# Kernel optimization log

Hardware: AMD Instinct MI355X
Metric: run time of the kernel (lower is better)

Reference implementation:

```python
import jax, jax.numpy as jnp
import numpy as np

B, N, F, P = 8, 16384, 128, 28


def setup_inputs() -> dict:
    key = jax.random.key(0)
    k1, k2 = jax.random.split(key)
    x = jax.random.uniform(k1, (B, N, 2), dtype=jnp.float32)  # 2D coords in [0,1]
    sigma = jnp.full((1,), np.log(0.05), dtype=jnp.float32)   # learned log-lengthscale
    image_features = jax.random.normal(k2, (F, P, P), dtype=jnp.float32) / np.sqrt(F)
    return {"x": x, "sigma": sigma, "image_features": image_features}


def reference(x, sigma, image_features):
    # x: [B, N, 2], sigma: [1] (log lengthscale), image_features: [F, P, P]
    P_ = image_features.shape[-1]
    grid = jnp.linspace(0.001, 1.0 - 0.001, P_, dtype=x.dtype)  # [P]
    ls = jnp.exp(sigma[0])                                      # lengthscale
    inv = 0.5 / (ls * ls)
    # pairwise squared dists grid vs each coordinate axis -> [B, P, N]
    d0 = (grid[None, :, None] - x[:, None, :, 0]) ** 2
    d1 = (grid[None, :, None] - x[:, None, :, 1]) ** 2
    k0 = jnp.exp(-inv * d0)  # [B, P, N]
    k1 = jnp.exp(-inv * d1)  # [B, P, N]
    # features[b,n,f] = sum_{p,q} k0[b,p,n] * IF[f,p,q] * k1[b,q,n]
    feats = jnp.einsum('bpn,fpq,bqn->bnf', k0, image_features, k1)
    return feats
```

## Files before the change

### kernel.cpp

```cpp
#include <hip/hip_runtime.h>

#define BDIM  8
#define NDIM  16384
#define FDIM  128
#define PDIM  28
#define KPAD  896
#define MPTS  (BDIM * NDIM)

typedef _Float16 half8  __attribute__((ext_vector_type(8)));
typedef float    floatx4 __attribute__((ext_vector_type(4)));

__global__ __launch_bounds__(256) void prep_ift(const float* __restrict__ IF,
                                                _Float16* __restrict__ IFt) {
    int idx = blockIdx.x * 256 + threadIdx.x;
    int f = idx / KPAD;
    int k = idx - f * KPAD;
    int p = k >> 5;
    int q = k & 31;
    float v = (q < PDIM) ? IF[f * (PDIM * PDIM) + p * PDIM + q] : 0.0f;
    IFt[idx] = (_Float16)v;
}

__global__ __launch_bounds__(256, 4) void feats_kernel(
    const float* __restrict__ x,
    const float* __restrict__ sigma,
    const _Float16* __restrict__ IFt,
    float* __restrict__ out)
{
    __shared__ float                 k0s[128 * 29];
    __shared__ __align__(16) _Float16 k1s[128 * 40];
    __shared__ __align__(16) _Float16 bs [128 * 40];

    const int tid  = threadIdx.x;
    const int lane = tid & 63;
    const int wave = tid >> 6;
    const int wm   = wave & 1;
    const int wn   = wave >> 1;
    const int ln15 = lane & 15;
    const int quad = lane >> 4;

    const float ls    = __expf(sigma[0]);
    const float inv   = 0.5f / (ls * ls);
    const float gstep = 0.998f / 27.0f;

    {
        const int ptl = tid & 127;
        const int ptg = blockIdx.x * 128 + ptl;
        if (tid < 128) {
            const float x0 = x[2 * ptg + 0];
            #pragma unroll
            for (int p = 0; p < PDIM; p++) {
                float d = (0.001f + p * gstep) - x0;
                k0s[ptl * 29 + p] = __expf(-inv * d * d);
            }
        } else {
            const float x1 = x[2 * ptg + 1];
            #pragma unroll
            for (int q = 0; q < PDIM; q++) {
                float d = (0.001f + q * gstep) - x1;
                k1s[ptl * 40 + q] = (_Float16)__expf(-inv * d * d);
            }
            #pragma unroll
            for (int q = PDIM; q < 32; q++)
                k1s[ptl * 40 + q] = (_Float16)0.0f;
        }
    }
    __syncthreads();

    half8 k1f[4];
    int   k0base[4];
    #pragma unroll
    for (int mt = 0; mt < 4; mt++) {
        const int mrow = wm * 64 + mt * 16 + ln15;
        k1f[mt]    = *(const half8*)&k1s[mrow * 40 + quad * 8];
        k0base[mt] = mrow * 29;
    }

    floatx4 acc[4][4];
    #pragma unroll
    for (int mt = 0; mt < 4; mt++)
        #pragma unroll
        for (int nt = 0; nt < 4; nt++)
            acc[mt][nt] = (floatx4){0.0f, 0.0f, 0.0f, 0.0f};

    const uint4* gI = (const uint4*)IFt;
    const int c0 = tid, c1 = tid + 256;
    const int f0 = c0 >> 2, cq0 = c0 & 3;
    const int f1 = c1 >> 2, cq1 = c1 & 3;
    uint4* bsw0 = (uint4*)&bs[f0 * 40 + cq0 * 8];
    uint4* bsw1 = (uint4*)&bs[f1 * 40 + cq1 * 8];
    uint4 pre0 = gI[f0 * 112 + cq0];
    uint4 pre1 = gI[f1 * 112 + cq1];

    #pragma unroll 1
    for (int kk = 0; kk < PDIM; kk++) {
        __syncthreads();
        *bsw0 = pre0;
        *bsw1 = pre1;
        if (kk < PDIM - 1) {
            pre0 = gI[f0 * 112 + (kk + 1) * 4 + cq0];
            pre1 = gI[f1 * 112 + (kk + 1) * 4 + cq1];
        }
        __syncthreads();

        half8 bf[4];
        #pragma unroll
        for (int nt = 0; nt < 4; nt++) {
            const int nrow = wn * 64 + nt * 16 + ln15;
            bf[nt] = *(const half8*)&bs[nrow * 40 + quad * 8];
        }

        #pragma unroll
        for (int mt = 0; mt < 4; mt++) {
            const float    k0v = k0s[k0base[mt] + kk];
            const _Float16 kh  = (_Float16)k0v;
            const half8    af  = k1f[mt] * kh;
            #pragma unroll
            for (int nt = 0; nt < 4; nt++) {
                acc[mt][nt] = __builtin_amdgcn_mfma_f32_16x16x32_f16(
                    af, bf[nt], acc[mt][nt], 0, 0, 0);
            }
        }
    }

    #pragma unroll
    for (int mt = 0; mt < 4; mt++) {
        const int row0 = blockIdx.x * 128 + wm * 64 + mt * 16 + quad * 4;
        #pragma unroll
        for (int nt = 0; nt < 4; nt++) {
            const int col = wn * 64 + nt * 16 + ln15;
            float* op = out + (size_t)row0 * FDIM + col;
            #pragma unroll
            for (int r = 0; r < 4; r++)
                __builtin_nontemporal_store(acc[mt][nt][r], op + (size_t)r * FDIM);
        }
    }
}

extern "C" void kernel_launch(void* const* d_in, const int* in_sizes, int n_in,
                              void* d_out, int out_size, void* d_ws, size_t ws_size,
                              hipStream_t stream) {
    const float* x     = (const float*)d_in[0];
    const float* sigma = (const float*)d_in[1];
    const float* IF    = (const float*)d_in[2];
    float* out = (float*)d_out;

    _Float16* IFt = (_Float16*)d_ws;

    prep_ift<<<(FDIM * KPAD) / 256, 256, 0, stream>>>(IF, IFt);
    feats_kernel<<<MPTS / 128, 256, 0, stream>>>(x, sigma, IFt, out);
}
```

Before: 102.2 us.

## Load IF operand fragments directly from global, drop shared staging and barriers

Removes the shared-memory staging buffer for the image-feature operand, along with the two barriers per k-step. Each wave now reads its own B fragments straight from global memory (expected to be L2-resident). The wave tiling changes from 2x2 to each wave covering all 128 points by 32 features, and k0 is stored as fp16 and read four k-steps at a time. This gives up some reuse of global loads across waves and raises register pressure (launch bounds lowered from 4 to 3), in exchange for fewer synchronisations and LDS round trips.

```diff
diff --git a/kernel.cpp b/kernel.cpp
--- a/kernel.cpp
+++ b/kernel.cpp
@@ -1,13 +1,12 @@
 #include <hip/hip_runtime.h>
 
-#define BDIM  8
-#define NDIM  16384
 #define FDIM  128
 #define PDIM  28
 #define KPAD  896
-#define MPTS  (BDIM * NDIM)
+#define MPTS  131072
 
-typedef _Float16 half8  __attribute__((ext_vector_type(8)));
+typedef _Float16 half8   __attribute__((ext_vector_type(8)));
+typedef _Float16 half4v  __attribute__((ext_vector_type(4)));
 typedef float    floatx4 __attribute__((ext_vector_type(4)));
 
 __global__ __launch_bounds__(256) void prep_ift(const float* __restrict__ IF,
@@ -21,21 +20,18 @@
     IFt[idx] = (_Float16)v;
 }
 
-__global__ __launch_bounds__(256, 4) void feats_kernel(
+__global__ __launch_bounds__(256, 3) void feats_kernel(
     const float* __restrict__ x,
     const float* __restrict__ sigma,
     const _Float16* __restrict__ IFt,
     float* __restrict__ out)
 {
-    __shared__ float                 k0s[128 * 29];
+    __shared__ _Float16               k0s[128 * 36];
     __shared__ __align__(16) _Float16 k1s[128 * 40];
-    __shared__ __align__(16) _Float16 bs [128 * 40];
 
     const int tid  = threadIdx.x;
     const int lane = tid & 63;
     const int wave = tid >> 6;
-    const int wm   = wave & 1;
-    const int wn   = wave >> 1;
     const int ln15 = lane & 15;
     const int quad = lane >> 4;
 
@@ -51,7 +47,7 @@
             #pragma unroll
             for (int p = 0; p < PDIM; p++) {
                 float d = (0.001f + p * gstep) - x0;
-                k0s[ptl * 29 + p] = __expf(-inv * d * d);
+                k0s[ptl * 36 + p] = (_Float16)__expf(-inv * d * d);
             }
         } else {
             const float x1 = x[2 * ptg + 1];
@@ -67,68 +63,58 @@
     }
     __syncthreads();
 
-    half8 k1f[4];
-    int   k0base[4];
+    half8 k1f[8];
     #pragma unroll
-    for (int mt = 0; mt < 4; mt++) {
-        const int mrow = wm * 64 + mt * 16 + ln15;
-        k1f[mt]    = *(const half8*)&k1s[mrow * 40 + quad * 8];
-        k0base[mt] = mrow * 29;
+    for (int mt = 0; mt < 8; mt++) {
+        const int m = mt * 16 + ln15;
+        k1f[mt] = *(const half8*)&k1s[m * 40 + quad * 8];
     }
 
-    floatx4 acc[4][4];
+    floatx4 acc[8][2];
     #pragma unroll
-    for (int mt = 0; mt < 4; mt++)
-        #pragma unroll
-        for (int nt = 0; nt < 4; nt++)
-            acc[mt][nt] = (floatx4){0.0f, 0.0f, 0.0f, 0.0f};
+    for (int mt = 0; mt < 8; mt++) {
+        acc[mt][0] = (floatx4){0.0f, 0.0f, 0.0f, 0.0f};
+        acc[mt][1] = (floatx4){0.0f, 0.0f, 0.0f, 0.0f};
+    }
 
-    const uint4* gI = (const uint4*)IFt;
-    const int c0 = tid, c1 = tid + 256;
-    const int f0 = c0 >> 2, cq0 = c0 & 3;
-    const int f1 = c1 >> 2, cq1 = c1 & 3;
-    uint4* bsw0 = (uint4*)&bs[f0 * 40 + cq0 * 8];
-    uint4* bsw1 = (uint4*)&bs[f1 * 40 + cq1 * 8];
-    uint4 pre0 = gI[f0 * 112 + cq0];
-    uint4 pre1 = gI[f1 * 112 + cq1];
+    const _Float16* gB0 = IFt + (size_t)(wave * 32 + ln15) * KPAD + quad * 8;
+    const _Float16* gB1 = gB0 + 16 * KPAD;
+
+    #define KSTEP(J)                                                          \
+    {                                                                         \
+        half8 bf0 = *(const half8*)(gB0 + kk4 * 128 + (J) * 32);              \
+        half8 bf1 = *(const half8*)(gB1 + kk4 * 128 + (J) * 32);              \
+        _Pragma("unroll")                                                     \
+        for (int mt = 0; mt < 8; mt++) {                                      \
+            const half8 af = k1f[mt] * k0v[mt][(J)];                          \
+            acc[mt][0] = __builtin_amdgcn_mfma_f32_16x16x32_f16(              \
+                af, bf0, acc[mt][0], 0, 0, 0);                                \
+            acc[mt][1] = __builtin_amdgcn_mfma_f32_16x16x32_f16(              \
+                af, bf1, acc[mt][1], 0, 0, 0);                                \
+        }                                                                     \
+    }
 
     #pragma unroll 1
-    for (int kk = 0; kk < PDIM; kk++) {
-        __syncthreads();
-        *bsw0 = pre0;
-        *bsw1 = pre1;
-        if (kk < PDIM - 1) {
-            pre0 = gI[f0 * 112 + (kk + 1) * 4 + cq0];
-            pre1 = gI[f1 * 112 + (kk + 1) * 4 + cq1];
+    for (int kk4 = 0; kk4 < 7; kk4++) {
+        half4v k0v[8];
+        #pragma unroll
+        for (int mt = 0; mt < 8; mt++) {
+            const int m = mt * 16 + ln15;
+            k0v[mt] = *(const half4v*)&k0s[m * 36 + kk4 * 4];
         }
-        __syncthreads();
-
-        half8 bf[4];
-        #pragma unroll
-        for (int nt = 0; nt < 4; nt++) {
-            const int nrow = wn * 64 + nt * 16 + ln15;
-            bf[nt] = *(const half8*)&bs[nrow * 40 + quad * 8];
-        }
-
-        #pragma unroll
-        for (int mt = 0; mt < 4; mt++) {
-            const float    k0v = k0s[k0base[mt] + kk];
-            const _Float16 kh  = (_Float16)k0v;
-            const half8    af  = k1f[mt] * kh;
-            #pragma unroll
-            for (int nt = 0; nt < 4; nt++) {
-                acc[mt][nt] = __builtin_amdgcn_mfma_f32_16x16x32_f16(
-                    af, bf[nt], acc[mt][nt], 0, 0, 0);
-            }
-        }
+        KSTEP(0)
+        KSTEP(1)
+        KSTEP(2)
+        KSTEP(3)
     }
+    #undef KSTEP
 
     #pragma unroll
-    for (int mt = 0; mt < 4; mt++) {
-        const int row0 = blockIdx.x * 128 + wm * 64 + mt * 16 + quad * 4;
+    for (int mt = 0; mt < 8; mt++) {
+        const int row0 = blockIdx.x * 128 + mt * 16 + quad * 4;
         #pragma unroll
-        for (int nt = 0; nt < 4; nt++) {
-            const int col = wn * 64 + nt * 16 + ln15;
+        for (int nt = 0; nt < 2; nt++) {
+            const int col = wave * 32 + nt * 16 + ln15;
             float* op = out + (size_t)row0 * FDIM + col;
             #pragma unroll
             for (int r = 0; r < 4; r++)
```

New measurement: 108.6 us. +6.3%, slower.
